# Kernel optimization log

Hardware: AMD Instinct MI355X
Metric: run time of the kernel (lower is better)

Reference implementation:

```python
import jax, jax.numpy as jnp
import numpy as np


def setup_inputs() -> dict:
    key = jax.random.key(0)
    k1, k2, k3, k4, k5, k6 = jax.random.split(key, 6)
    B, V = 128, 128000
    logits = jax.random.normal(k1, (B, V), dtype=jnp.float32) * 2.0
    # keep temperatures away from 0 to avoid overflow in logits/temp
    temperatures = 0.7 + 0.6 * jax.random.uniform(k2, (B,), dtype=jnp.float32)
    top_ks = jax.random.randint(k3, (B,), 1, 1024, dtype=jnp.int32)
    top_ps = 0.7 + 0.29 * jax.random.uniform(k4, (B,), dtype=jnp.float32)
    min_ps = 0.02 * jax.random.uniform(k5, (B,), dtype=jnp.float32)
    # uniform variate for inverse-CDF multinomial sampling (one sample per row)
    u = jax.random.uniform(k6, (B, 1), dtype=jnp.float32)
    return {
        "logits": logits,
        "temperatures": temperatures,
        "top_ks": top_ks,
        "top_ps": top_ps,
        "min_ps": min_ps,
        "u": u,
    }


def reference(logits, temperatures, top_ks, top_ps, min_ps, u):
    """Faithful jax version of Sampler's torch-native sampling path:
    softmax(logits/T) -> descending sort -> top-k mask -> top-p mask
    (cumsum computed pre-mask, exactly as torch code) -> min-p mask ->
    multinomial sample (inverse CDF with provided uniform u) ->
    gather original token index. Also returns the renormalized filtered
    probs scattered back to vocab order (top_p_normalize_probs-style)."""
    B, V = logits.shape
    probs = jax.nn.softmax(logits / temperatures[:, None], axis=-1)  # [B, V]

    order = jnp.argsort(-probs, axis=-1)                     # descending indices
    probs_sort = jnp.take_along_axis(probs, order, axis=-1)  # [B, V] sorted desc
    probs_sum = jnp.cumsum(probs_sort, axis=-1)              # cumsum BEFORE masking

    pos = jnp.arange(V, dtype=jnp.int32)[None, :]
    # top-k: zero everything at rank >= top_k
    probs_sort = jnp.where(pos >= top_ks[:, None], 0.0, probs_sort)
    # top-p: zero where cumulative mass strictly before this token exceeds top_p
    probs_sort = jnp.where(probs_sum - probs_sort > top_ps[:, None], 0.0, probs_sort)
    # min-p: threshold relative to the max prob (rank-0 entry survives both masks)
    min_p_thr = probs_sort[:, :1] * min_ps[:, None]
    probs_sort = jnp.where(probs_sort < min_p_thr, 0.0, probs_sort)

    total = jnp.sum(probs_sort, axis=-1, keepdims=True)      # [B, 1]
    cdf = jnp.cumsum(probs_sort, axis=-1) / total            # normalized CDF
    # inverse-CDF sampling == torch.multinomial(probs_sort, 1)
    sampled_rank = jnp.clip(jnp.sum(cdf < u, axis=-1, keepdims=True), 0, V - 1)
    token_ids = jnp.take_along_axis(order, sampled_rank, axis=-1)[:, 0].astype(jnp.int32)

    # scatter renormalized filtered probs back to original vocab positions
    inv_order = jnp.argsort(order, axis=-1)
    norm_probs = jnp.take_along_axis(probs_sort / total, inv_order, axis=-1)
    return token_ids, norm_probs
```

## Files before the change

### kernel.cpp

```cpp
#include <hip/hip_runtime.h>
#include <stdint.h>
#include <math.h>

#define TPB 1024
#define NB 2048
#define SPLIT 4
#define LCAND 2560
#define CAND2 2048
#define PS 4096
#define L2E 1.44269504088896f

typedef float vfloat4 __attribute__((ext_vector_type(4)));
typedef unsigned long long ull;

__device__ __forceinline__ unsigned fkey(float f) {
    unsigned u = __float_as_uint(f);
    return (u & 0x80000000u) ? ~u : (u | 0x80000000u);
}
__device__ __forceinline__ float funkey(unsigned k) {
    unsigned u = (k & 0x80000000u) ? (k ^ 0x80000000u) : ~k;
    return __uint_as_float(u);
}
__device__ __forceinline__ ull packkv(unsigned k, unsigned idx) {
    return ((ull)k << 32) | (ull)(~idx);
}

__device__ __forceinline__ void suffix_scan_2048(unsigned* h, unsigned* wscr, int tid)
{
    const int lane = tid & 63, w = tid >> 6;
    const int i0 = 2047 - 2 * tid;
    const int i1 = 2046 - 2 * tid;
    unsigned a = h[i0], b = h[i1];
    unsigned s = a + b;
    unsigned inc = s;
    #pragma unroll
    for (int d = 1; d < 64; d <<= 1) { unsigned o = __shfl_up(inc, d); if (lane >= d) inc += o; }
    if (lane == 63) wscr[w] = inc;
    __syncthreads();
    if (w == 0) {
        unsigned v = (lane < 16) ? wscr[lane] : 0u;
        unsigned vi = v;
        #pragma unroll
        for (int d = 1; d < 16; d <<= 1) { unsigned o = __shfl_up(vi, d); if (lane >= d) vi += o; }
        if (lane < 16) wscr[16 + lane] = vi - v;
    }
    __syncthreads();
    unsigned off = wscr[16 + w] + (inc - s);
    h[i0] = off + a;
    h[i1] = off + a + b;
    __syncthreads();
}

__global__ __launch_bounds__(TPB)
void k1_scan(const float* __restrict__ logits,
             const float* __restrict__ temps,
             const int* __restrict__ top_ks,
             float* __restrict__ out_probs,
             float* __restrict__ ws_meta,
             unsigned* __restrict__ ws_cut,
             unsigned* __restrict__ ws_cnt,
             ull* __restrict__ ws_cand,
             int V, int Vq)
{
    const int sblk = blockIdx.x;
    const int b = sblk / SPLIT, s = sblk % SPLIT;
    const int tid = threadIdx.x, lane = tid & 63, w = tid >> 6;
    const int start = s * Vq;
    const int len = min(Vq, V - start);
    const int slot = sblk;
    const float invT = 1.0f / temps[b];
    int K = top_ks[b]; K = max(K, 1); K = min(K, 1024);

    __shared__ unsigned hist[NB];
    __shared__ unsigned uscr[32];
    __shared__ float fred[32];
    __shared__ unsigned cnt;
    __shared__ int bstar;

    if (len <= 0) {
        if (tid == 0) {
            ws_meta[2*slot] = -1e30f; ws_meta[2*slot+1] = 0.0f;
            ws_cut[slot] = 0xFFFFFFFFu; ws_cnt[slot] = 0u;
        }
        return;
    }

    for (int i = tid; i < NB; i += TPB) hist[i] = 0;
    if (tid == 0) { cnt = 0; bstar = 0; }
    __syncthreads();

    const float* __restrict__ row = logits + (size_t)b * V + start;
    const vfloat4* __restrict__ row4 = (const vfloat4*)row;
    const int L4 = len >> 2;

    const int nps = min(len, PS);
    float m0 = -1e30f;
    for (int i = tid; i < nps; i += TPB) {
        float lv = row[i];
        m0 = fmaxf(m0, lv);
        atomicAdd(&hist[fkey(lv) >> 21], 1u);
    }
    #pragma unroll
    for (int d = 32; d > 0; d >>= 1) m0 = fmaxf(m0, __shfl_down(m0, d));
    if (lane == 0) fred[w] = m0;
    __syncthreads();
    if (tid == 0) {
        float mm = fred[0];
        for (int j = 1; j < 16; ++j) mm = fmaxf(mm, fred[j]);
        fred[16] = mm;
    }
    __syncthreads();
    const float m0max = fred[16];

    suffix_scan_2048(hist, uscr, tid);
    float sexp = (float)K * (float)nps / (float)V;
    unsigned TGT = (unsigned)(sexp + 6.0f * sqrtf(sexp) + 16.5f);
    if (TGT > (unsigned)nps) TGT = (unsigned)nps;
    for (int e = tid; e < NB; e += TPB) {
        unsigned Se = hist[e];
        unsigned Sn = (e < NB - 1) ? hist[e + 1] : 0u;
        if (Se >= TGT && Sn < TGT) bstar = e;
    }
    __syncthreads();
    const unsigned cutkey = (unsigned)bstar << 21;
    const float cutval = funkey(cutkey);

    {
        float* __restrict__ orow = out_probs + (size_t)b * V + start;
        vfloat4* __restrict__ orow4 = (vfloat4*)orow;
        const vfloat4 z4 = (vfloat4)0.0f;
        for (int i = tid; i < L4; i += TPB) __builtin_nontemporal_store(z4, &orow4[i]);
        for (int i = (L4 << 2) + tid; i < len; i += TPB) __builtin_nontemporal_store(0.0f, &orow[i]);
    }

    const float ca = invT * L2E;
    const float cb = -m0max * invT * L2E;
    ull* gc = ws_cand + (size_t)slot * LCAND;

    float z0 = 0.0f, z1 = 0.0f, z2 = 0.0f, z3 = 0.0f;

    #define E4(v) (exp2f(fmaf((v)[0], ca, cb)) + exp2f(fmaf((v)[1], ca, cb)) \
                 + exp2f(fmaf((v)[2], ca, cb)) + exp2f(fmaf((v)[3], ca, cb)))
    #define GATHER(v, ii) do {                                                  \
        bool c0 = (v)[0] >= cutval, c1 = (v)[1] >= cutval,                      \
             c2 = (v)[2] >= cutval, c3 = (v)[3] >= cutval;                      \
        if (c0 | c1 | c2 | c3) {                                                \
            int nh = (int)c0 + (int)c1 + (int)c2 + (int)c3;                     \
            unsigned base = atomicAdd(&cnt, (unsigned)nh);                      \
            unsigned bi = (unsigned)(start + ((ii) << 2));                      \
            if (c0) { if (base < LCAND) gc[base] = packkv(fkey((v)[0]), bi+0); base++; } \
            if (c1) { if (base < LCAND) gc[base] = packkv(fkey((v)[1]), bi+1); base++; } \
            if (c2) { if (base < LCAND) gc[base] = packkv(fkey((v)[2]), bi+2); base++; } \
            if (c3) { if (base < LCAND) gc[base] = packkv(fkey((v)[3]), bi+3); base++; } \
        }                                                                       \
    } while (0)

    int i = tid;
    for (; i + 3 * TPB < L4; i += 4 * TPB) {
        vfloat4 va = row4[i];
        vfloat4 vb = row4[i + TPB];
        vfloat4 vc = row4[i + 2 * TPB];
        vfloat4 vd = row4[i + 3 * TPB];
        z0 += E4(va); z1 += E4(vb); z2 += E4(vc); z3 += E4(vd);
        GATHER(va, i); GATHER(vb, i + TPB); GATHER(vc, i + 2 * TPB); GATHER(vd, i + 3 * TPB);
    }
    for (; i < L4; i += TPB) {
        vfloat4 v = row4[i];
        z0 += E4(v);
        GATHER(v, i);
    }
    for (int j = (L4 << 2) + tid; j < len; j += TPB) {
        float lv = row[j];
        z0 += exp2f(fmaf(lv, ca, cb));
        if (lv >= cutval) {
            unsigned base = atomicAdd(&cnt, 1u);
            if (base < LCAND) gc[base] = packkv(fkey(lv), (unsigned)(start + j));
        }
    }
    #undef E4
    #undef GATHER

    float z = (z0 + z1) + (z2 + z3);
    __syncthreads();
    #pragma unroll
    for (int d = 32; d > 0; d >>= 1) z += __shfl_down(z, d);
    if (lane == 0) fred[w] = z;
    __syncthreads();
    if (tid == 0) {
        float zz = 0.0f;
        for (int j = 0; j < 16; ++j) zz += fred[j];
        ws_meta[2*slot + 0] = m0max * invT;
        ws_meta[2*slot + 1] = zz;
        ws_cut[slot] = cutkey;
        ws_cnt[slot] = cnt;
    }
}

__global__ __launch_bounds__(TPB)
void k2_sample(const float* __restrict__ logits,
               const float* __restrict__ temps,
               const int* __restrict__ top_ks,
               const float* __restrict__ top_ps,
               const float* __restrict__ min_ps,
               const float* __restrict__ uvec,
               const float* __restrict__ ws_meta,
               const unsigned* __restrict__ ws_cut,
               const unsigned* __restrict__ ws_cnt,
               const ull* __restrict__ ws_cand,
               float* __restrict__ out_tok,
               float* __restrict__ out_probs,
               int V)
{
    const int b = blockIdx.x;
    const int tid = threadIdx.x, lane = tid & 63, w = tid >> 6;
    const float invT = 1.0f / temps[b];
    int Korig = top_ks[b]; Korig = max(Korig, 1); Korig = min(Korig, 1024);
    const unsigned Ku = (unsigned)Korig;
    const float top_p = top_ps[b], min_p = min_ps[b], uval = uvec[b];

    __shared__ __align__(16) char smem[53504];
    ull*            cand  = (ull*)(smem);
    ull*            cand2 = (ull*)(smem + 16384);
    unsigned*       hist  = (unsigned*)(smem + 32768);
    unsigned short* cnts  = (unsigned short*)(smem + 41216);
    float*          sh_p  = (float*)(smem + 45312);
    float*          sh_c  = (float*)(smem + 49408);
    __shared__ unsigned uscr[32];
    __shared__ float fws[32];
    __shared__ unsigned scnt, sh_mk;
    __shared__ int sh_i1, sh_i2;
    __shared__ unsigned sh_u1;

    float Cy[SPLIT], zq[SPLIT];
    unsigned cutq[SPLIT], cntq[SPLIT];
    #pragma unroll
    for (int q = 0; q < SPLIT; ++q) {
        int sl = b * SPLIT + q;
        Cy[q] = ws_meta[2*sl]; zq[q] = ws_meta[2*sl+1];
        cutq[q] = ws_cut[sl]; cntq[q] = ws_cnt[sl];
    }
    float Y = -1e30f;
    #pragma unroll
    for (int q = 0; q < SPLIT; ++q) if (cntq[q] > 0u) Y = fmaxf(Y, Cy[q]);
    float Z = 0.0f;
    #pragma unroll
    for (int q = 0; q < SPLIT; ++q)
        if (cntq[q] > 0u && zq[q] > 0.0f) Z += zq[q] * exp2f((Cy[q] - Y) * L2E);

    bool fb = false;
    unsigned cutmax = 0, mincut = 0xFFFFFFFFu;
    #pragma unroll
    for (int q = 0; q < SPLIT; ++q) {
        if (cntq[q] > (unsigned)LCAND) fb = true;
        if (cntq[q] > 0u) {
            if (!isfinite(zq[q])) fb = true;
            cutmax = max(cutmax, cutq[q]);
            mincut = min(mincut, cutq[q]);
        }
    }
    if (mincut == 0xFFFFFFFFu || !isfinite(Z) || Z <= 0.0f) fb = true;

    unsigned Tkeyb = 0;
    int count = 0, bstar = 0, shift = 0;
    unsigned base = mincut;

    if (!fb) {
        unsigned mk = 0;
        if (tid == 0) sh_mk = 0;
        for (int i = tid; i <= NB; i += TPB) hist[i] = 0;
        if (tid == 0) { sh_i1 = -1; scnt = 0; }
        __syncthreads();
        #pragma unroll
        for (int q = 0; q < SPLIT; ++q) {
            const ull* gc = ws_cand + (size_t)(b * SPLIT + q) * LCAND;
            int nl = min((int)cntq[q], LCAND);
            for (int i = tid; i < nl; i += TPB)
                mk = max(mk, (unsigned)(gc[i] >> 32));
        }
        #pragma unroll
        for (int d = 32; d > 0; d >>= 1) mk = max(mk, __shfl_down(mk, d));
        if (lane == 0) atomicMax(&sh_mk, mk);
        __syncthreads();
        const unsigned maxkey = sh_mk;
        const unsigned range = maxkey - base;
        while ((range >> shift) > (unsigned)(NB - 1)) shift++;

        #pragma unroll
        for (int q = 0; q < SPLIT; ++q) {
            const ull* gc = ws_cand + (size_t)(b * SPLIT + q) * LCAND;
            int nl = min((int)cntq[q], LCAND);
            for (int i = tid; i < nl; i += TPB)
                atomicAdd(&hist[((unsigned)(gc[i] >> 32) - base) >> shift], 1u);
        }
        __syncthreads();
        unsigned fat = 0;
        for (int i = tid; i < NB; i += TPB) {
            unsigned h = hist[i];
            cnts[i] = (unsigned short)h;
            fat = max(fat, h);
        }
        #pragma unroll
        for (int d = 32; d > 0; d >>= 1) fat = max(fat, __shfl_down(fat, d));
        if (lane == 0) uscr[w] = fat;
        __syncthreads();
        if (tid == 0) {
            unsigned m2 = 0;
            for (int j = 0; j < 16; ++j) m2 = max(m2, uscr[j]);
            uscr[16] = m2;
        }
        __syncthreads();
        if (uscr[16] > 64u) fb = true;
    }
    if (!fb) {
        suffix_scan_2048(hist, uscr, tid);
        for (int e = tid; e < NB; e += TPB) {
            unsigned Se = hist[e], Sn = (e < NB - 1) ? hist[e + 1] : 0u;
            if (Se >= Ku && Sn < Ku) { sh_i1 = e; sh_u1 = Se; }
        }
        __syncthreads();
        if (sh_i1 < 0) fb = true;
        else {
            bstar = sh_i1;
            count = (int)sh_u1;
            Tkeyb = base + ((unsigned)bstar << shift);
            if (Tkeyb < cutmax || count > CAND2) fb = true;
        }
    }
    if (!fb) {
        #pragma unroll
        for (int q = 0; q < SPLIT; ++q) {
            const ull* gc = ws_cand + (size_t)(b * SPLIT + q) * LCAND;
            int nl = min((int)cntq[q], LCAND);
            for (int i = tid; i < nl; i += TPB) {
                ull e = gc[i];
                unsigned k = (unsigned)(e >> 32);
                if (k >= Tkeyb) {
                    unsigned bin = (k - base) >> shift;
                    unsigned pos = atomicAdd(&hist[bin + 1], 1u);
                    cand2[pos] = e;
                }
            }
        }
        __syncthreads();
        for (int e = bstar + tid; e < NB; e += TPB) {
            int c = (int)cnts[e];
            if (c >= 2) {
                int st = (int)hist[e + 1] - c;
                for (int x = 1; x < c; ++x) {
                    ull key = cand2[st + x];
                    int y = x - 1;
                    while (y >= 0 && cand2[st + y] < key) { cand2[st + y + 1] = cand2[st + y]; --y; }
                    cand2[st + y + 1] = key;
                }
            }
        }
        __syncthreads();
    }

    if (fb) {
        const float* __restrict__ row = logits + (size_t)b * V;
        float m = -1e30f, z = 0.0f;
        for (int i = tid; i < V; i += TPB) {
            float y = row[i] * invT;
            float nm = fmaxf(m, y);
            z = z * exp2f((m - nm) * L2E) + exp2f((y - nm) * L2E);
            m = nm;
        }
        sh_p[tid] = m; sh_c[tid] = z;
        __syncthreads();
        for (int d = TPB >> 1; d > 0; d >>= 1) {
            if (tid < d) {
                float m1 = sh_p[tid], z1 = sh_c[tid];
                float m2 = sh_p[tid + d], z2 = sh_c[tid + d];
                float mm = fmaxf(m1, m2);
                sh_c[tid] = z1 * exp2f((m1 - mm) * L2E) + z2 * exp2f((m2 - mm) * L2E);
                sh_p[tid] = mm;
            }
            __syncthreads();
        }
        Y = sh_p[0]; Z = sh_c[0];
        __syncthreads();
        for (int i = tid; i < NB; i += TPB) hist[i] = 0;
        if (tid == 0) { sh_i1 = 0; sh_i2 = 0; sh_u1 = 0; }
        __syncthreads();
        for (int i = tid; i < V; i += TPB) atomicAdd(&hist[fkey(row[i]) >> 21], 1u);
        __syncthreads();
        suffix_scan_2048(hist, uscr, tid);
        for (int e = tid; e < NB; e += TPB) {
            unsigned Se = hist[e], Sn = (e < NB-1) ? hist[e+1] : 0u;
            if (Se >= Ku && Sn < Ku) { sh_i1 = e; sh_u1 = Sn; }
        }
        __syncthreads();
        int b1 = sh_i1;
        unsigned cab = sh_u1;
        for (int i = tid; i < NB; i += TPB) hist[i] = 0;
        __syncthreads();
        for (int i = tid; i < V; i += TPB) {
            unsigned k = fkey(row[i]);
            if ((int)(k >> 21) == b1) atomicAdd(&hist[(k >> 10) & (NB - 1)], 1u);
        }
        __syncthreads();
        suffix_scan_2048(hist, uscr, tid);
        for (int e = tid; e < NB; e += TPB) {
            unsigned Se = cab + hist[e];
            unsigned Sn = cab + ((e < NB-1) ? hist[e+1] : 0u);
            if (Se >= Ku && Sn < Ku) sh_i2 = e;
        }
        __syncthreads();
        unsigned Tkey = ((unsigned)b1 << 21) | ((unsigned)sh_i2 << 10);
        if (tid == 0) scnt = 0;
        __syncthreads();
        for (int i = tid; i < V; i += TPB) {
            unsigned k = fkey(row[i]);
            if (k >= Tkey) {
                unsigned pos = atomicAdd(&scnt, 1u);
                if (pos < CAND2) cand[pos] = packkv(k, (unsigned)i);
            }
        }
        __syncthreads();
        count = (scnt < (unsigned)CAND2) ? (int)scnt : CAND2;

        int n_sort = 1;
        while (n_sort < count) n_sort <<= 1;
        for (int i = tid; i < n_sort; i += TPB)
            if (i >= count) cand[i] = 0ull;
        __syncthreads();
        for (int kk = 2; kk <= n_sort; kk <<= 1) {
            for (int j = kk >> 1; j > 0; j >>= 1) {
                for (int i = tid; i < n_sort; i += TPB) {
                    int ixj = i ^ j;
                    if (ixj > i) {
                        ull a = cand[i], c = cand[ixj];
                        bool up = (i & kk) == 0;
                        if (up ? (a < c) : (a > c)) { cand[i] = c; cand[ixj] = a; }
                    }
                }
                __syncthreads();
            }
        }
    }

    ull* srt = fb ? cand : cand2;
    int K = min(Korig, count);

    float pv = 0.0f;
    if (tid < K) {
        unsigned k = (unsigned)(srt[tid] >> 32);
        pv = exp2f((funkey(k) * invT - Y) * L2E) / Z;
    }
    float inc = pv;
    #pragma unroll
    for (int d = 1; d < 64; d <<= 1) { float o = __shfl_up(inc, d); if (lane >= d) inc += o; }
    if (lane == 63) fws[w] = inc;
    __syncthreads();
    if (w == 0) {
        float v = (lane < 16) ? fws[lane] : 0.0f;
        float vi = v;
        #pragma unroll
        for (int d = 1; d < 16; d <<= 1) { float o = __shfl_up(vi, d); if (lane >= d) vi += o; }
        if (lane < 16) fws[16 + lane] = vi - v;
    }
    __syncthreads();
    float cum = inc + fws[16 + w];
    sh_p[tid] = pv;
    sh_c[tid] = cum;
    if (tid == 0) sh_i1 = K;
    __syncthreads();

    if (tid < K) {
        float excl = cum - pv;
        if (excl > top_p) atomicMin(&sh_i1, tid);
    }
    __syncthreads();
    int n1 = sh_i1;
    float thr = sh_p[0] * min_p;
    if (tid == 0) sh_i2 = n1;
    __syncthreads();
    if (tid < n1 && sh_p[tid] < thr) atomicMin(&sh_i2, tid);
    __syncthreads();
    int nf = sh_i2;
    float total = sh_c[nf - 1];

    int pred = (tid < nf) && ((sh_c[tid] / total) < uval);
    int rank = __syncthreads_count(pred);
    if (rank > nf - 1) rank = nf - 1;
    if (rank < 0) rank = 0;
    if (tid == 0)
        out_tok[b] = (float)(~(unsigned)(srt[rank] & 0xFFFFFFFFull));

    if (tid < nf) {
        unsigned idx = ~(unsigned)(srt[tid] & 0xFFFFFFFFull);
        out_probs[(size_t)b * V + idx] = sh_p[tid] / total;
    }
}

extern "C" void kernel_launch(void* const* d_in, const int* in_sizes, int n_in,
                              void* d_out, int out_size, void* d_ws, size_t ws_size,
                              hipStream_t stream) {
    const float* logits = (const float*)d_in[0];
    const float* temps  = (const float*)d_in[1];
    const int*   top_ks = (const int*)d_in[2];
    const float* top_ps = (const float*)d_in[3];
    const float* min_ps = (const float*)d_in[4];
    const float* u      = (const float*)d_in[5];
    const int B = in_sizes[1];
    const int V = in_sizes[0] / B;
    float* out_tok   = (float*)d_out;
    float* out_probs = out_tok + B;

    int Vq = (((V + SPLIT - 1) / SPLIT) + 3) & ~3;

    char* ws = (char*)d_ws;
    size_t off = 0;
    auto take = [&](size_t bytes) { char* p = ws + off; off = (off + bytes + 255) & ~(size_t)255; return p; };
    float*    ws_meta = (float*)take((size_t)B * SPLIT * 2 * sizeof(float));
    unsigned* ws_cut  = (unsigned*)take((size_t)B * SPLIT * sizeof(unsigned));
    unsigned* ws_cnt  = (unsigned*)take((size_t)B * SPLIT * sizeof(unsigned));
    ull*      ws_cand = (ull*)take((size_t)B * SPLIT * LCAND * sizeof(ull));
    (void)ws_size;

    k1_scan<<<dim3(SPLIT * B), dim3(TPB), 0, stream>>>(
        logits, temps, top_ks, out_probs, ws_meta, ws_cut, ws_cnt, ws_cand, V, Vq);
    k2_sample<<<dim3(B), dim3(TPB), 0, stream>>>(
        logits, temps, top_ks, top_ps, min_ps, u, ws_meta, ws_cut, ws_cnt, ws_cand,
        out_tok, out_probs, V);
}
```

Baseline: 151.4 us.

## Fuse output zeroing into logit scan and compute per-slice max key in k1

In k1, the histogram prefix pass now reads exactly one vector per thread and reuses it later, so that chunk is not loaded twice. Zeroing of the output row is interleaved with the main streaming loop, and loads use nontemporal hints. k1 also tracks the maximum logit key per slice and writes it to a new workspace buffer. This lets k2 skip a full extra pass over the candidate lists plus a block barrier. The cost is more code paths and extra register pressure from the additional max accumulators.

New measurement: 154.3 us. Within noise of the previous version (+1.9%).

```diff
diff --git a/kernel.cpp b/kernel.cpp
--- a/kernel.cpp
+++ b/kernel.cpp
@@ -59,6 +59,7 @@
              float* __restrict__ ws_meta,
              unsigned* __restrict__ ws_cut,
              unsigned* __restrict__ ws_cnt,
+             unsigned* __restrict__ ws_max,
              ull* __restrict__ ws_cand,
              int V, int Vq)
 {
@@ -80,7 +81,7 @@
     if (len <= 0) {
         if (tid == 0) {
             ws_meta[2*slot] = -1e30f; ws_meta[2*slot+1] = 0.0f;
-            ws_cut[slot] = 0xFFFFFFFFu; ws_cnt[slot] = 0u;
+            ws_cut[slot] = 0xFFFFFFFFu; ws_cnt[slot] = 0u; ws_max[slot] = 0u;
         }
         return;
     }
@@ -91,14 +92,29 @@
 
     const float* __restrict__ row = logits + (size_t)b * V + start;
     const vfloat4* __restrict__ row4 = (const vfloat4*)row;
+    float* __restrict__ orow = out_probs + (size_t)b * V + start;
+    vfloat4* __restrict__ orow4 = (vfloat4*)orow;
+    const vfloat4 z4 = (vfloat4)0.0f;
     const int L4 = len >> 2;
-
-    const int nps = min(len, PS);
+    const bool vec = (len >= 4 * TPB);
+    const int nps = vec ? (4 * TPB) : min(len, PS);
+
     float m0 = -1e30f;
-    for (int i = tid; i < nps; i += TPB) {
-        float lv = row[i];
-        m0 = fmaxf(m0, lv);
-        atomicAdd(&hist[fkey(lv) >> 21], 1u);
+    vfloat4 pv = z4;
+    if (vec) {
+        pv = __builtin_nontemporal_load(&row4[tid]);
+        __builtin_nontemporal_store(z4, &orow4[tid]);
+        m0 = fmaxf(fmaxf(pv[0], pv[1]), fmaxf(pv[2], pv[3]));
+        atomicAdd(&hist[fkey(pv[0]) >> 21], 1u);
+        atomicAdd(&hist[fkey(pv[1]) >> 21], 1u);
+        atomicAdd(&hist[fkey(pv[2]) >> 21], 1u);
+        atomicAdd(&hist[fkey(pv[3]) >> 21], 1u);
+    } else {
+        for (int i = tid; i < nps; i += TPB) {
+            float lv = row[i];
+            m0 = fmaxf(m0, lv);
+            atomicAdd(&hist[fkey(lv) >> 21], 1u);
+        }
     }
     #pragma unroll
     for (int d = 32; d > 0; d >>= 1) m0 = fmaxf(m0, __shfl_down(m0, d));
@@ -125,10 +141,7 @@
     const unsigned cutkey = (unsigned)bstar << 21;
     const float cutval = funkey(cutkey);
 
-    {
-        float* __restrict__ orow = out_probs + (size_t)b * V + start;
-        vfloat4* __restrict__ orow4 = (vfloat4*)orow;
-        const vfloat4 z4 = (vfloat4)0.0f;
+    if (!vec) {
         for (int i = tid; i < L4; i += TPB) __builtin_nontemporal_store(z4, &orow4[i]);
         for (int i = (L4 << 2) + tid; i < len; i += TPB) __builtin_nontemporal_store(0.0f, &orow[i]);
     }
@@ -138,9 +151,11 @@
     ull* gc = ws_cand + (size_t)slot * LCAND;
 
     float z0 = 0.0f, z1 = 0.0f, z2 = 0.0f, z3 = 0.0f;
+    float mA = m0, mB = -1e30f, mC = -1e30f, mD = -1e30f;
 
     #define E4(v) (exp2f(fmaf((v)[0], ca, cb)) + exp2f(fmaf((v)[1], ca, cb)) \
                  + exp2f(fmaf((v)[2], ca, cb)) + exp2f(fmaf((v)[3], ca, cb)))
+    #define M4(v) fmaxf(fmaxf((v)[0], (v)[1]), fmaxf((v)[2], (v)[3]))
     #define GATHER(v, ii) do {                                                  \
         bool c0 = (v)[0] >= cutval, c1 = (v)[1] >= cutval,                      \
              c2 = (v)[2] >= cutval, c3 = (v)[3] >= cutval;                      \
@@ -155,44 +170,92 @@
         }                                                                       \
     } while (0)
 
-    int i = tid;
-    for (; i + 3 * TPB < L4; i += 4 * TPB) {
-        vfloat4 va = row4[i];
-        vfloat4 vb = row4[i + TPB];
-        vfloat4 vc = row4[i + 2 * TPB];
-        vfloat4 vd = row4[i + 3 * TPB];
-        z0 += E4(va); z1 += E4(vb); z2 += E4(vc); z3 += E4(vd);
-        GATHER(va, i); GATHER(vb, i + TPB); GATHER(vc, i + 2 * TPB); GATHER(vd, i + 3 * TPB);
-    }
-    for (; i < L4; i += TPB) {
-        vfloat4 v = row4[i];
-        z0 += E4(v);
-        GATHER(v, i);
-    }
-    for (int j = (L4 << 2) + tid; j < len; j += TPB) {
-        float lv = row[j];
-        z0 += exp2f(fmaf(lv, ca, cb));
-        if (lv >= cutval) {
-            unsigned base = atomicAdd(&cnt, 1u);
-            if (base < LCAND) gc[base] = packkv(fkey(lv), (unsigned)(start + j));
+    if (vec) {
+        int i = TPB + tid;
+        for (; i + 3 * TPB < L4; i += 4 * TPB) {
+            vfloat4 va = __builtin_nontemporal_load(&row4[i]);
+            vfloat4 vb = __builtin_nontemporal_load(&row4[i + TPB]);
+            vfloat4 vc = __builtin_nontemporal_load(&row4[i + 2 * TPB]);
+            vfloat4 vd = __builtin_nontemporal_load(&row4[i + 3 * TPB]);
+            __builtin_nontemporal_store(z4, &orow4[i]);
+            __builtin_nontemporal_store(z4, &orow4[i + TPB]);
+            __builtin_nontemporal_store(z4, &orow4[i + 2 * TPB]);
+            __builtin_nontemporal_store(z4, &orow4[i + 3 * TPB]);
+            z0 += E4(va); z1 += E4(vb); z2 += E4(vc); z3 += E4(vd);
+            mA = fmaxf(mA, M4(va)); mB = fmaxf(mB, M4(vb));
+            mC = fmaxf(mC, M4(vc)); mD = fmaxf(mD, M4(vd));
+            GATHER(va, i); GATHER(vb, i + TPB); GATHER(vc, i + 2 * TPB); GATHER(vd, i + 3 * TPB);
+        }
+        for (; i < L4; i += TPB) {
+            vfloat4 v = __builtin_nontemporal_load(&row4[i]);
+            __builtin_nontemporal_store(z4, &orow4[i]);
+            z0 += E4(v);
+            mA = fmaxf(mA, M4(v));
+            GATHER(v, i);
+        }
+        for (int j = (L4 << 2) + tid; j < len; j += TPB) {
+            float lv = row[j];
+            __builtin_nontemporal_store(0.0f, &orow[j]);
+            z0 += exp2f(fmaf(lv, ca, cb));
+            mA = fmaxf(mA, lv);
+            if (lv >= cutval) {
+                unsigned base = atomicAdd(&cnt, 1u);
+                if (base < LCAND) gc[base] = packkv(fkey(lv), (unsigned)(start + j));
+            }
+        }
+        z0 += E4(pv);
+        GATHER(pv, tid);
+    } else {
+        int i = tid;
+        for (; i + 3 * TPB < L4; i += 4 * TPB) {
+            vfloat4 va = row4[i];
+            vfloat4 vb = row4[i + TPB];
+            vfloat4 vc = row4[i + 2 * TPB];
+            vfloat4 vd = row4[i + 3 * TPB];
+            z0 += E4(va); z1 += E4(vb); z2 += E4(vc); z3 += E4(vd);
+            mA = fmaxf(mA, M4(va)); mB = fmaxf(mB, M4(vb));
+            mC = fmaxf(mC, M4(vc)); mD = fmaxf(mD, M4(vd));
+            GATHER(va, i); GATHER(vb, i + TPB); GATHER(vc, i + 2 * TPB); GATHER(vd, i + 3 * TPB);
+        }
+        for (; i < L4; i += TPB) {
+            vfloat4 v = row4[i];
+            z0 += E4(v);
+            mA = fmaxf(mA, M4(v));
+            GATHER(v, i);
+        }
+        for (int j = (L4 << 2) + tid; j < len; j += TPB) {
+            float lv = row[j];
+            z0 += exp2f(fmaf(lv, ca, cb));
+            mA = fmaxf(mA, lv);
+            if (lv >= cutval) {
+                unsigned base = atomicAdd(&cnt, 1u);
+                if (base < LCAND) gc[base] = packkv(fkey(lv), (unsigned)(start + j));
+            }
         }
     }
     #undef E4
+    #undef M4
     #undef GATHER
 
     float z = (z0 + z1) + (z2 + z3);
-    __syncthreads();
-    #pragma unroll
-    for (int d = 32; d > 0; d >>= 1) z += __shfl_down(z, d);
-    if (lane == 0) fred[w] = z;
+    unsigned rk = fkey(fmaxf(fmaxf(mA, mB), fmaxf(mC, mD)));
+    __syncthreads();
+    #pragma unroll
+    for (int d = 32; d > 0; d >>= 1) {
+        z += __shfl_down(z, d);
+        rk = max(rk, __shfl_down(rk, d));
+    }
+    if (lane == 0) { fred[w] = z; uscr[w] = rk; }
     __syncthreads();
     if (tid == 0) {
         float zz = 0.0f;
-        for (int j = 0; j < 16; ++j) zz += fred[j];
+        unsigned mk = 0u;
+        for (int j = 0; j < 16; ++j) { zz += fred[j]; mk = max(mk, uscr[j]); }
         ws_meta[2*slot + 0] = m0max * invT;
         ws_meta[2*slot + 1] = zz;
         ws_cut[slot] = cutkey;
         ws_cnt[slot] = cnt;
+        ws_max[slot] = mk;
     }
 }
 
@@ -206,6 +269,7 @@
                const float* __restrict__ ws_meta,
                const unsigned* __restrict__ ws_cut,
                const unsigned* __restrict__ ws_cnt,
+               const unsigned* __restrict__ ws_max,
                const ull* __restrict__ ws_cand,
                float* __restrict__ out_tok,
                float* __restrict__ out_probs,
@@ -227,17 +291,17 @@
     float*          sh_c  = (float*)(smem + 49408);
     __shared__ unsigned uscr[32];
     __shared__ float fws[32];
-    __shared__ unsigned scnt, sh_mk;
+    __shared__ unsigned scnt;
     __shared__ int sh_i1, sh_i2;
     __shared__ unsigned sh_u1;
 
     float Cy[SPLIT], zq[SPLIT];
-    unsigned cutq[SPLIT], cntq[SPLIT];
+    unsigned cutq[SPLIT], cntq[SPLIT], mxq[SPLIT];
     #pragma unroll
     for (int q = 0; q < SPLIT; ++q) {
         int sl = b * SPLIT + q;
         Cy[q] = ws_meta[2*sl]; zq[q] = ws_meta[2*sl+1];
-        cutq[q] = ws_cut[sl]; cntq[q] = ws_cnt[sl];
+        cutq[q] = ws_cut[sl]; cntq[q] = ws_cnt[sl]; mxq[q] = ws_max[sl];
     }
     float Y = -1e30f;
     #pragma unroll
@@ -265,25 +329,15 @@
     unsigned base = mincut;
 
     if (!fb) {
-        unsigned mk = 0;
-        if (tid == 0) sh_mk = 0;
         for (int i = tid; i <= NB; i += TPB) hist[i] = 0;
-        if (tid == 0) { sh_i1 = -1; scnt = 0; }
-        __syncthreads();
+        if (tid == 0) sh_i1 = -1;
+        unsigned maxkey = 0;
         #pragma unroll
-        for (int q = 0; q < SPLIT; ++q) {
-            const ull* gc = ws_cand + (size_t)(b * SPLIT + q) * LCAND;
-            int nl = min((int)cntq[q], LCAND);
-            for (int i = tid; i < nl; i += TPB)
-                mk = max(mk, (unsigned)(gc[i] >> 32));
-        }
-        #pragma unroll
-        for (int d = 32; d > 0; d >>= 1) mk = max(mk, __shfl_down(mk, d));
-        if (lane == 0) atomicMax(&sh_mk, mk);
-        __syncthreads();
-        const unsigned maxkey = sh_mk;
+        for (int q = 0; q < SPLIT; ++q)
+            if (cntq[q] > 0u) maxkey = max(maxkey, mxq[q]);
         const unsigned range = maxkey - base;
         while ((range >> shift) > (unsigned)(NB - 1)) shift++;
+        __syncthreads();
 
         #pragma unroll
         for (int q = 0; q < SPLIT; ++q) {
@@ -516,12 +570,13 @@
     float*    ws_meta = (float*)take((size_t)B * SPLIT * 2 * sizeof(float));
     unsigned* ws_cut  = (unsigned*)take((size_t)B * SPLIT * sizeof(unsigned));
     unsigned* ws_cnt  = (unsigned*)take((size_t)B * SPLIT * sizeof(unsigned));
+    unsigned* ws_maxk = (unsigned*)take((size_t)B * SPLIT * sizeof(unsigned));
     ull*      ws_cand = (ull*)take((size_t)B * SPLIT * LCAND * sizeof(ull));
     (void)ws_size;
 
     k1_scan<<<dim3(SPLIT * B), dim3(TPB), 0, stream>>>(
-        logits, temps, top_ks, out_probs, ws_meta, ws_cut, ws_cnt, ws_cand, V, Vq);
+        logits, temps, top_ks, out_probs, ws_meta, ws_cut, ws_cnt, ws_maxk, ws_cand, V, Vq);
     k2_sample<<<dim3(B), dim3(TPB), 0, stream>>>(
-        logits, temps, top_ks, top_ps, min_ps, u, ws_meta, ws_cut, ws_cnt, ws_cand,
+        logits, temps, top_ks, top_ps, min_ps, u, ws_meta, ws_cut, ws_cnt, ws_maxk, ws_cand,
         out_tok, out_probs, V);
 }
```
